# Performance work log

Measured on AMD Instinct MI355X. Metric: run time of the kernel, lower is better.

## Reference

```python
import jax, jax.numpy as jnp
import numpy as np

N_NODES = 50000
N_EDGES = 800000
IN_DIM, HID_DIM, OUT_DIM = 256, 256, 128


def gcn_conv(x, edge_index, W, b, num_nodes):
    """PyG GCNConv: self-loops + symmetric norm + linear + scatter-add + bias."""
    loop = jnp.arange(num_nodes, dtype=edge_index.dtype)
    src = jnp.concatenate([edge_index[0], loop])  # message sources
    dst = jnp.concatenate([edge_index[1], loop])  # message targets
    ones = jnp.ones(dst.shape[0], dtype=x.dtype)
    deg = jax.ops.segment_sum(ones, dst, num_segments=num_nodes)
    dinv = jnp.where(deg > 0, jax.lax.rsqrt(deg), 0.0)
    norm = dinv[src] * dinv[dst]                  # [E+N]
    h = x @ W                                     # [N, out]
    msg = h[src] * norm[:, None]                  # gather + scale, [E+N, out]
    out = jax.ops.segment_sum(msg, dst, num_segments=num_nodes)
    return out + b


def setup_inputs() -> dict:
    key = jax.random.key(0)
    k1, k2, k3, k4, k5, k6 = jax.random.split(key, 6)
    x = jax.random.normal(k1, (N_NODES, IN_DIM), dtype=jnp.float32)
    edge_index = jax.random.randint(k2, (2, N_EDGES), 0, N_NODES, dtype=jnp.int64)
    s1 = 1.0 / np.sqrt(IN_DIM)
    s2 = 1.0 / np.sqrt(HID_DIM)
    W1 = jax.random.uniform(k3, (IN_DIM, HID_DIM), jnp.float32, -s1, s1)
    b1 = jax.random.uniform(k4, (HID_DIM,), jnp.float32, -s1, s1)
    W2 = jax.random.uniform(k5, (HID_DIM, OUT_DIM), jnp.float32, -s2, s2)
    b2 = jax.random.uniform(k6, (OUT_DIM,), jnp.float32, -s2, s2)
    return {"x": x, "edge_index": edge_index, "W1": W1, "b1": b1, "W2": W2, "b2": b2}


def reference(x, edge_index, W1, b1, W2, b2):
    n = x.shape[0]
    h = jax.nn.relu(gcn_conv(x, edge_index, W1, b1, n))
    out = jax.nn.sigmoid(gcn_conv(h, edge_index, W2, b2, n))
    return out
```

## Files before the change

### kernel.cpp

```cpp
#include <hip/hip_runtime.h>
#include <hip/hip_bf16.h>
#include <math.h>

#define N_NODES 50000
#define N_EDGES 800000
#define D_IN 256
#define D_HID 256
#define D_OUT 128

typedef unsigned short ushort_t;
typedef unsigned char uchar_t;
typedef __attribute__((ext_vector_type(8))) short bf16x8;
typedef __attribute__((ext_vector_type(4))) float f32x4;

__device__ inline ushort_t f2bf(float f) {
    __hip_bfloat16 h = __float2bfloat16(f);
    return *reinterpret_cast<ushort_t*>(&h);
}
__device__ inline uchar_t f2fp8(float a) {
    int w = __builtin_amdgcn_cvt_pk_fp8_f32(a, a, 0, false);
    return (uchar_t)(w & 0xff);
}
__device__ inline void fp8x4_to_f32(unsigned u, float* o) {
    auto p0 = __builtin_amdgcn_cvt_pk_f32_fp8(u, false);
    auto p1 = __builtin_amdgcn_cvt_pk_f32_fp8(u, true);
    o[0] = p0[0]; o[1] = p0[1]; o[2] = p1[0]; o[3] = p1[1];
}
__device__ inline void fp8x2_to_f32(unsigned u, float* o) {
    auto p0 = __builtin_amdgcn_cvt_pk_f32_fp8(u, false);
    o[0] = p0[0]; o[1] = p0[1];
}

#define NODES_PER_GRP 6250


__global__ __launch_bounds__(256) void k_count_convW(const int* __restrict__ dst,
                                                     int* __restrict__ degI,
                                                     const float* __restrict__ W1,
                                                     const float* __restrict__ W2,
                                                     ushort_t* __restrict__ Wt1,
                                                     ushort_t* __restrict__ Wt2,
                                                     uchar_t* __restrict__ h1z,
                                                     uchar_t* __restrict__ h2z) {
    const int b = blockIdx.x;
    if (b < 512) {
        const int g = b & 7;
        const int slice = b >> 3;
        const int lo = g * NODES_PER_GRP, hi = lo + NODES_PER_GRP;
        const int i0 = slice * 12500;
        for (int i = i0 + threadIdx.x; i < i0 + 12500; i += 256) {
            const int d = dst[i];
            if (d >= lo && d < hi) atomicAdd(&degI[d], 1);
        }
    } else {
        int i = (b - 512) * 256 + threadIdx.x;
        const int n1 = D_IN * D_HID;
        const int n2 = D_HID * D_OUT;
        if (i < n1) {
            int k = i / D_HID, n = i % D_HID;
            Wt1[(size_t)n * D_IN + k] = f2bf(W1[i]);
        } else if (i < n1 + n2) {
            int j = i - n1;
            int k = j / D_OUT, n = j % D_OUT;
            Wt2[(size_t)n * D_HID + k] = f2bf(W2[j]);
        } else {
            int j = i - n1 - n2;
            if (j < D_HID) h1z[j] = 0;
            else if (j < D_HID + D_OUT) h2z[j - D_HID] = 0;
        }
    }
}


__global__ __launch_bounds__(256) void k_scan_apply(const int* __restrict__ degI,
                                                    int* __restrict__ offs,
                                                    int* __restrict__ cursor,
                                                    float* __restrict__ dinv,
                                                    ushort_t* __restrict__ ebuf, int n) {
    __shared__ int s[256];
    const int t = threadIdx.x;
    const int b = blockIdx.x;

    int pre = 0;
    const int lim = b * 256;
    for (int i = t; i < lim; i += 256) pre += (degI[i] + 15) & ~15;
    s[t] = pre;
    __syncthreads();
    for (int st = 128; st > 0; st >>= 1) {
        if (t < st) s[t] += s[t + st];
        __syncthreads();
    }
    const int blockoff = s[0];
    __syncthreads();

    const int i = b * 256 + t;
    const int deg = (i < n) ? degI[i] : 0;
    const int v = (deg + 15) & ~15;
    s[t] = v;
    __syncthreads();
    for (int off = 1; off < 256; off <<= 1) {
        int u = 0;
        if (t >= off) u = s[t - off];
        __syncthreads();
        if (t >= off) s[t] += u;
        __syncthreads();
    }
    const int excl = s[t] - v + blockoff;
    if (i < n) {
        offs[i] = excl;
        cursor[i] = excl;
        dinv[i] = rsqrtf((float)(1 + deg));
        for (int p = excl + deg; p < excl + v; ++p) ebuf[p] = (ushort_t)N_NODES;
        if (i == n - 1) offs[n] = excl + v;
    }
}


__global__ __launch_bounds__(512) void k_fill_gemm1(const int* __restrict__ src,
                                                    const int* __restrict__ dst,
                                                    int* __restrict__ cursor,
                                                    ushort_t* __restrict__ ebuf,
                                                    const float* __restrict__ A,
                                                    const ushort_t* __restrict__ Bt,
                                                    const float* __restrict__ dinvD,
                                                    uchar_t* __restrict__ C,
                                                    int M, int gemmBlocks) {
    __shared__ ushort_t As[128 * 40];
    __shared__ ushort_t Bs[256 * 40];

    if (blockIdx.x >= gemmBlocks) {
        const int fb = blockIdx.x - gemmBlocks;
        const int g = fb & 7;
        const int slice = fb >> 3;
        const int lo = g * NODES_PER_GRP, hi = lo + NODES_PER_GRP;
        const int i0 = slice * 4000;
        for (int i = i0 + threadIdx.x; i < i0 + 4000; i += 512) {
            const int d = dst[i];
            if (d >= lo && d < hi) {
                const int pos = atomicAdd(&cursor[d], 1);
                ebuf[pos] = (ushort_t)src[i];
            }
        }
        return;
    }

    const int t = threadIdx.x;
    const int lane = t & 63;
    const int w = t >> 6;
    const int wr = w >> 2;
    const int wc = w & 3;
    const int m0 = blockIdx.x * 128;

    const int arow = t >> 2;
    const int acol = (t & 3) * 8;
    const int brow = t >> 1;
    const int bcol = (t & 1) * 16;

    f32x4 acc[4][4];
#pragma unroll
    for (int m = 0; m < 4; ++m)
#pragma unroll
        for (int n = 0; n < 4; ++n)
#pragma unroll
            for (int i = 0; i < 4; ++i) acc[m][n][i] = 0.0f;

    for (int kt = 0; kt < 256; kt += 32) {
        {
            const int gr = m0 + arow;
            float4 v0 = make_float4(0.f, 0.f, 0.f, 0.f);
            float4 v1 = make_float4(0.f, 0.f, 0.f, 0.f);
            if (gr < M) {
                const float* p = A + (size_t)gr * 256 + kt + acol;
                v0 = *(const float4*)p;
                v1 = *(const float4*)(p + 4);
            }
            ushort4 u0, u1;
            u0.x = f2bf(v0.x); u0.y = f2bf(v0.y); u0.z = f2bf(v0.z); u0.w = f2bf(v0.w);
            u1.x = f2bf(v1.x); u1.y = f2bf(v1.y); u1.z = f2bf(v1.z); u1.w = f2bf(v1.w);
            *(ushort4*)&As[arow * 40 + acol] = u0;
            *(ushort4*)&As[arow * 40 + acol + 4] = u1;
        }
        {
            const uint4* p = (const uint4*)(Bt + (size_t)brow * 256 + kt + bcol);
            uint4 v0 = p[0], v1 = p[1];
            *(uint4*)&Bs[brow * 40 + bcol] = v0;
            *(uint4*)&Bs[brow * 40 + bcol + 8] = v1;
        }
        __syncthreads();

        const int kg = (lane >> 4) * 8;
        const int lr = lane & 15;
        bf16x8 a[4], b[4];
#pragma unroll
        for (int m = 0; m < 4; ++m)
            a[m] = *(const bf16x8*)&As[(wr * 64 + m * 16 + lr) * 40 + kg];
#pragma unroll
        for (int n = 0; n < 4; ++n)
            b[n] = *(const bf16x8*)&Bs[(wc * 64 + n * 16 + lr) * 40 + kg];
#pragma unroll
        for (int m = 0; m < 4; ++m)
#pragma unroll
            for (int n = 0; n < 4; ++n)
                acc[m][n] = __builtin_amdgcn_mfma_f32_16x16x32_bf16(a[m], b[n], acc[m][n], 0, 0, 0);
        __syncthreads();
    }

    const int lr = lane & 15;
    const int rg = (lane >> 4) * 4;
#pragma unroll
    for (int m = 0; m < 4; ++m) {
        const int rb = m0 + wr * 64 + m * 16 + rg;
#pragma unroll
        for (int i = 0; i < 4; ++i) {
            const int row = rb + i;
            if (row < M) {
                const float dr = dinvD[row];
#pragma unroll
                for (int n = 0; n < 4; ++n) {
                    const int col = wc * 64 + n * 16 + lr;
                    C[(size_t)row * 256 + col] = f2fp8(acc[m][n][i] * dr);
                }
            }
        }
    }
}


__device__ inline void ld_idx16u(const ushort_t* __restrict__ p, int* s) {
    uint4 a = ((const uint4*)p)[0];
    uint4 b = ((const uint4*)p)[1];
    unsigned w0 = __builtin_amdgcn_readfirstlane(a.x);
    unsigned w1 = __builtin_amdgcn_readfirstlane(a.y);
    unsigned w2 = __builtin_amdgcn_readfirstlane(a.z);
    unsigned w3 = __builtin_amdgcn_readfirstlane(a.w);
    unsigned w4 = __builtin_amdgcn_readfirstlane(b.x);
    unsigned w5 = __builtin_amdgcn_readfirstlane(b.y);
    unsigned w6 = __builtin_amdgcn_readfirstlane(b.z);
    unsigned w7 = __builtin_amdgcn_readfirstlane(b.w);
    s[0]  = w0 & 0xffff; s[1]  = w0 >> 16;
    s[2]  = w1 & 0xffff; s[3]  = w1 >> 16;
    s[4]  = w2 & 0xffff; s[5]  = w2 >> 16;
    s[6]  = w3 & 0xffff; s[7]  = w3 >> 16;
    s[8]  = w4 & 0xffff; s[9]  = w4 >> 16;
    s[10] = w5 & 0xffff; s[11] = w5 >> 16;
    s[12] = w6 & 0xffff; s[13] = w6 >> 16;
    s[14] = w7 & 0xffff; s[15] = w7 >> 16;
}


__global__ __launch_bounds__(512) void k_agg_gemm2(const uchar_t* __restrict__ h,
                                                   const float* __restrict__ dinv,
                                                   const int* __restrict__ offs,
                                                   const ushort_t* __restrict__ ebuf,
                                                   const float* __restrict__ bias,
                                                   const ushort_t* __restrict__ Bt,
                                                   uchar_t* __restrict__ h2, int n) {
    __shared__ ushort_t As[64 * 264];
    __shared__ ushort_t Bs[128 * 40];

    const int t = threadIdx.x;
    const int lane = t & 63;
    const int w = t >> 6;
    const int m0 = blockIdx.x * 64;

    const int base = lane * 4;
    const uchar_t* hb = h + base;

    for (int i = 0; i < 8; ++i) {
        const int row = w * 8 + i;
        const int node = m0 + row;
        if (node < n) {
            float acc[4];
            {
                const unsigned u = *(const unsigned*)(hb + (size_t)node * D_HID);
                fp8x4_to_f32(u, acc);
            }
            int e = __builtin_amdgcn_readfirstlane(offs[node]);
            const int e1 = __builtin_amdgcn_readfirstlane(offs[node + 1]);
            int cs[16], ns[16];
            bool have = e < e1;
            if (have) ld_idx16u(ebuf + e, cs);
            while (have) {
                const int en = e + 16;
                const bool hn = en < e1;
                unsigned u[16];
#pragma unroll
                for (int j = 0; j < 16; ++j)
                    u[j] = *(const unsigned*)(hb + (size_t)cs[j] * D_HID);
                if (hn) ld_idx16u(ebuf + en, ns);
#pragma unroll
                for (int j = 0; j < 16; ++j) {
                    float d[4];
                    fp8x4_to_f32(u[j], d);
                    acc[0] += d[0]; acc[1] += d[1]; acc[2] += d[2]; acc[3] += d[3];
                }
                e = en; have = hn;
#pragma unroll
                for (int j = 0; j < 16; ++j) cs[j] = ns[j];
            }
            const float di = dinv[node];
            ushort4 o;
            o.x = f2bf(fmaxf(di * acc[0] + bias[base + 0], 0.f));
            o.y = f2bf(fmaxf(di * acc[1] + bias[base + 1], 0.f));
            o.z = f2bf(fmaxf(di * acc[2] + bias[base + 2], 0.f));
            o.w = f2bf(fmaxf(di * acc[3] + bias[base + 3], 0.f));
            *(ushort4*)&As[row * 264 + base] = o;
        }
    }
    __syncthreads();

    const int lr = lane & 15;
    const int kg = (lane >> 4) * 8;

    f32x4 acc2[4];
#pragma unroll
    for (int m = 0; m < 4; ++m)
#pragma unroll
        for (int i = 0; i < 4; ++i) acc2[m][i] = 0.0f;

    for (int kt = 0; kt < 256; kt += 32) {
        {
            const int srow = t >> 2;
            const int scol = (t & 3) * 8;
            const uint4* p = (const uint4*)(Bt + (size_t)srow * 256 + kt + scol);
            *(uint4*)&Bs[srow * 40 + scol] = p[0];
        }
        __syncthreads();

        bf16x8 a[4], b;
#pragma unroll
        for (int m = 0; m < 4; ++m)
            a[m] = *(const bf16x8*)&As[(m * 16 + lr) * 264 + kt + kg];
        b = *(const bf16x8*)&Bs[(w * 16 + lr) * 40 + kg];
#pragma unroll
        for (int m = 0; m < 4; ++m)
            acc2[m] = __builtin_amdgcn_mfma_f32_16x16x32_bf16(a[m], b, acc2[m], 0, 0, 0);
        __syncthreads();
    }

    const int rg = (lane >> 4) * 4;
#pragma unroll
    for (int m = 0; m < 4; ++m) {
#pragma unroll
        for (int i = 0; i < 4; ++i) {
            const int gr = m0 + m * 16 + rg + i;
            if (gr < n) {
                const int col = w * 16 + lr;
                h2[(size_t)gr * 128 + col] = f2fp8(acc2[m][i] * dinv[gr]);
            }
        }
    }
}


__global__ __launch_bounds__(256) void k_gather_fp8_2(const uchar_t* __restrict__ h,
                                                      const float* __restrict__ dinv,
                                                      const int* __restrict__ offs,
                                                      const ushort_t* __restrict__ ebuf,
                                                      const float* __restrict__ bias,
                                                      float* __restrict__ out, int n) {
    const int node = (blockIdx.x * 256 + threadIdx.x) >> 6;
    const int lane = threadIdx.x & 63;
    if (node >= n) return;

    const int base = lane * 2;
    const uchar_t* hb = h + base;
    const float di = dinv[node];

    float acc[2];
    {
        const unsigned u = *(const ushort_t*)(hb + (size_t)node * D_OUT);
        fp8x2_to_f32(u, acc);
    }

    int e = __builtin_amdgcn_readfirstlane(offs[node]);
    const int e1 = __builtin_amdgcn_readfirstlane(offs[node + 1]);

    int cs[16], ns[16];
    bool have = e < e1;
    if (have) ld_idx16u(ebuf + e, cs);

    while (have) {
        const int en = e + 16;
        const bool hn = en < e1;
        unsigned u[16];
#pragma unroll
        for (int j = 0; j < 16; ++j)
            u[j] = *(const ushort_t*)(hb + (size_t)cs[j] * D_OUT);
        if (hn) ld_idx16u(ebuf + en, ns);
#pragma unroll
        for (int j = 0; j < 16; ++j) {
            float d[2];
            fp8x2_to_f32(u[j], d);
            acc[0] += d[0]; acc[1] += d[1];
        }
        e = en; have = hn;
#pragma unroll
        for (int j = 0; j < 16; ++j) cs[j] = ns[j];
    }

    const float v0 = di * acc[0] + bias[base + 0];
    const float v1 = di * acc[1] + bias[base + 1];
    float2 r;
    r.x = 1.0f / (1.0f + expf(-v0));
    r.y = 1.0f / (1.0f + expf(-v1));
    *(float2*)(out + (size_t)node * D_OUT + base) = r;
}


extern "C" void kernel_launch(void* const* d_in, const int* in_sizes, int n_in,
                              void* d_out, int out_size, void* d_ws, size_t ws_size,
                              hipStream_t stream) {
    const float* x  = (const float*)d_in[0];
    const int*   ei = (const int*)d_in[1];
    const float* W1 = (const float*)d_in[2];
    const float* b1 = (const float*)d_in[3];
    const float* W2 = (const float*)d_in[4];
    const float* b2 = (const float*)d_in[5];
    float* out = (float*)d_out;

    float* wsf    = (float*)d_ws;
    float* dinv   = wsf;
    int*   degI   = (int*)(wsf + 50048);
    int*   offs   = degI + 50048;
    int*   cursor = offs + 50064;
    ushort_t* ebuf= (ushort_t*)(cursor + 50048);
    ushort_t* Wt1 = ebuf + 1600000;
    ushort_t* Wt2 = Wt1 + 65536;
    uchar_t*  h1  = (uchar_t*)(Wt2 + 32768);
    uchar_t*  h2  = h1 + (size_t)50048 * D_HID;

    const int* src = ei;
    const int* dst = ei + N_EDGES;

    const int blocksN = (N_NODES + 255) / 256;

    hipMemsetAsync(degI, 0, N_NODES * sizeof(int), stream);

    k_count_convW<<<512 + 386, 256, 0, stream>>>(dst, degI, W1, W2, Wt1, Wt2,
                                                 h1 + (size_t)N_NODES * D_HID,
                                                 h2 + (size_t)N_NODES * D_OUT);

    k_scan_apply<<<blocksN, 256, 0, stream>>>(degI, offs, cursor, dinv, ebuf, N_NODES);

    {
        const int gemmBlocks = (N_NODES + 127) / 128;
        k_fill_gemm1<<<gemmBlocks + 1600, 512, 0, stream>>>(
            src, dst, cursor, ebuf, x, Wt1, dinv, h1, N_NODES, gemmBlocks);
    }

    k_agg_gemm2<<<(N_NODES + 63) / 64, 512, 0, stream>>>(
        h1, dinv, offs, ebuf, b1, Wt2, h2, N_NODES);

    k_gather_fp8_2<<<(N_NODES * 64 + 255) / 256, 256, 0, stream>>>(
        h2, dinv, offs, ebuf, b2, out, N_NODES);
}
```

Before: 210.0 us.

## Use LDS-local cursors for CSR fill with per-block destination ranges

The edge-fill phase is restructured so that each of 64 blocks owns a contiguous range of destination nodes and keeps its insertion cursors in shared memory instead of global memory. Each block streams the entire dst array with vectorized int4 loads and performs LDS atomics for matching edges. The global cursor array and its initialization in the scan kernel are removed. This trades contended global atomics for many more redundant reads of dst per block, with fewer fill blocks that may lengthen the tail alongside the GEMM blocks.

New measurement: 496.8 us. 137% more time.

```diff
diff --git a/kernel.cpp b/kernel.cpp
--- a/kernel.cpp
+++ b/kernel.cpp
@@ -32,6 +32,8 @@
 }
 
 #define NODES_PER_GRP 6250
+#define FILL_GROUPS 64
+#define FILL_NPG 782
 
 
 __global__ __launch_bounds__(256) void k_count_convW(const int* __restrict__ dst,
@@ -74,7 +76,6 @@
 
 __global__ __launch_bounds__(256) void k_scan_apply(const int* __restrict__ degI,
                                                     int* __restrict__ offs,
-                                                    int* __restrict__ cursor,
                                                     float* __restrict__ dinv,
                                                     ushort_t* __restrict__ ebuf, int n) {
     __shared__ int s[256];
@@ -108,7 +109,6 @@
     const int excl = s[t] - v + blockoff;
     if (i < n) {
         offs[i] = excl;
-        cursor[i] = excl;
         dinv[i] = rsqrtf((float)(1 + deg));
         for (int p = excl + deg; p < excl + v; ++p) ebuf[p] = (ushort_t)N_NODES;
         if (i == n - 1) offs[n] = excl + v;
@@ -118,7 +118,7 @@
 
 __global__ __launch_bounds__(512) void k_fill_gemm1(const int* __restrict__ src,
                                                     const int* __restrict__ dst,
-                                                    int* __restrict__ cursor,
+                                                    const int* __restrict__ offs,
                                                     ushort_t* __restrict__ ebuf,
                                                     const float* __restrict__ A,
                                                     const ushort_t* __restrict__ Bt,
@@ -129,16 +129,26 @@
     __shared__ ushort_t Bs[256 * 40];
 
     if (blockIdx.x >= gemmBlocks) {
-        const int fb = blockIdx.x - gemmBlocks;
-        const int g = fb & 7;
-        const int slice = fb >> 3;
-        const int lo = g * NODES_PER_GRP, hi = lo + NODES_PER_GRP;
-        const int i0 = slice * 4000;
-        for (int i = i0 + threadIdx.x; i < i0 + 4000; i += 512) {
-            const int d = dst[i];
-            if (d >= lo && d < hi) {
-                const int pos = atomicAdd(&cursor[d], 1);
-                ebuf[pos] = (ushort_t)src[i];
+        const int g = blockIdx.x - gemmBlocks;
+        const int lo = g * FILL_NPG;
+        const int hi = min(lo + FILL_NPG, M);
+        const int npg = hi - lo;
+        int* lcur = (int*)As;
+        for (int j = threadIdx.x; j < npg; j += 512)
+            lcur[j] = offs[lo + j];
+        __syncthreads();
+
+        const int4* d4 = (const int4*)dst;
+        for (int ii = threadIdx.x; ii < N_EDGES / 4; ii += 512) {
+            const int4 dv = d4[ii];
+            const int bi = ii * 4;
+#pragma unroll
+            for (int k = 0; k < 4; ++k) {
+                const int d = (&dv.x)[k];
+                if (d >= lo && d < hi) {
+                    const int pos = atomicAdd(&lcur[d - lo], 1);
+                    ebuf[pos] = (ushort_t)src[bi + k];
+                }
             }
         }
         return;
@@ -441,12 +451,12 @@
                                                  h1 + (size_t)N_NODES * D_HID,
                                                  h2 + (size_t)N_NODES * D_OUT);
 
-    k_scan_apply<<<blocksN, 256, 0, stream>>>(degI, offs, cursor, dinv, ebuf, N_NODES);
+    k_scan_apply<<<blocksN, 256, 0, stream>>>(degI, offs, dinv, ebuf, N_NODES);
 
     {
         const int gemmBlocks = (N_NODES + 127) / 128;
-        k_fill_gemm1<<<gemmBlocks + 1600, 512, 0, stream>>>(
-            src, dst, cursor, ebuf, x, Wt1, dinv, h1, N_NODES, gemmBlocks);
+        k_fill_gemm1<<<gemmBlocks + FILL_GROUPS, 512, 0, stream>>>(
+            src, dst, offs, ebuf, x, Wt1, dinv, h1, N_NODES, gemmBlocks);
     }
 
     k_agg_gemm2<<<(N_NODES + 63) / 64, 512, 0, stream>>>(
```
